# Kernel tuning notes

Hardware: AMD Instinct MI355X
Metric: run time of the kernel (lower is better)

## Reference

```python
import jax, jax.numpy as jnp
import numpy as np

B, SIZE, E = 256, 64, 4096
DEPTH = 2
ADDITIONAL = 16


def _forward(input, keys, offset, sampled_bits):
    b, s, e = input.shape
    m = SIZE >> DEPTH  # section size at this depth
    # choices: first row = round(offset), rest = sampled bits  -> (b, n, s)
    first = jax.lax.stop_gradient(jnp.round(offset)).astype(jnp.int32)[:, None, :]
    choices = jnp.concatenate([first, sampled_bits.astype(jnp.int32)], axis=1)
    n = choices.shape[1]
    # probability of each full choice vector: prod_i (offset_i if c_i else 1-offset_i)
    off = offset[:, None, :]  # (b,1,s)
    p = jnp.where(choices == 1, off, 1.0 - off)  # (b,n,s)
    probs = jnp.prod(p, axis=2, keepdims=True)  # (b,n,1)
    probs = probs / jnp.sum(probs, axis=1, keepdims=True)
    probs = jnp.broadcast_to(probs, (b, n, s))
    # util.split: element at position i (section sec, in-section pos pin) goes to
    # top half (pin//2) or bottom half (m//2 + pin//2) of its section.
    i = jnp.arange(s)
    sec = (i // m) * m
    pin = i % m
    out0 = sec + pin // 2
    out1 = sec + m // 2 + pin // 2
    indices = jnp.where(choices == 1, out1[None, None, :], out0[None, None, :])  # (b,n,s)
    # duplicates: choice rows determine index rows bijectively, so compare choice rows.
    # mark all occurrences except the first (matches stable-sort-based dedup).
    eq = jnp.all(choices[:, :, None, :] == choices[:, None, :, :], axis=-1)  # (b,n,n)
    earlier = jnp.triu(jnp.ones((n, n), dtype=bool), 1)  # mask_{i,j}: i < j
    dups = jnp.any(eq & earlier[None], axis=1)  # (b,n)
    probs = jnp.where(dups[:, :, None], 0.0, probs)
    # batched sparse matmul via dense scatter of the (s,s) matrix per batch
    rows = indices.reshape(b, -1)  # (b, n*s)
    cols = jnp.broadcast_to(i[None, None, :], (b, n, s)).reshape(b, -1)
    vals = probs.reshape(b, -1).astype(input.dtype)
    bidx = jnp.arange(b)[:, None]
    M = jnp.zeros((b, s, s), input.dtype).at[bidx, rows, cols].add(vals)  # (b,s,s)
    output = jnp.einsum('brc,bce->bre', M, input)  # (b,s,e)
    keys_out = jnp.einsum('brc,bc->br', M, keys)   # (b,s)
    return output, keys_out


def setup_inputs() -> dict:
    key = jax.random.key(0)
    k1, k2, k3, k4 = jax.random.split(key, 4)
    return {
        'input': jax.random.normal(k1, (B, SIZE, E), jnp.float32),
        'keys': jax.random.normal(k2, (B, SIZE), jnp.float32),
        'offset': jax.random.uniform(k3, (B, SIZE), jnp.float32),
        'sampled_bits': jax.random.randint(k4, (B, ADDITIONAL, SIZE), 0, 2, jnp.int32),
    }


def reference(input, keys, offset, sampled_bits):
    return _forward(input, keys, offset, sampled_bits)
```

## Files before the change

### kernel.cpp

```cpp
#include <hip/hip_runtime.h>

#define BB     256
#define S      64
#define EE     4096
#define NROWS  17

typedef float f32x4 __attribute__((ext_vector_type(4)));

__global__ __launch_bounds__(64) void split_weights_kernel(
    const float* __restrict__ keys,
    const float* __restrict__ offset,
    const int*   __restrict__ bits,
    float* __restrict__ W0,
    float* __restrict__ W1,
    float* __restrict__ keys_out)
{
    const int b    = blockIdx.x;
    const int lane = threadIdx.x;

    __shared__ float              s_off[S];
    __shared__ unsigned long long s_mask[NROWS];
    __shared__ float              s_prob[NROWS];
    __shared__ float              s_W0[S], s_W1[S];
    __shared__ float              s_sum;

    const float off = offset[b * S + lane];
    s_off[lane] = off;

    unsigned long long m = __ballot((int)rintf(off) == 1);
    if (lane == 0) s_mask[0] = m;
    for (int j = 0; j < NROWS - 1; ++j) {
        const int bit = bits[((size_t)b * (NROWS - 1) + j) * S + lane];
        m = __ballot(bit == 1);
        if (lane == 0) s_mask[1 + j] = m;
    }
    __syncthreads();

    if (lane < NROWS) {
        const unsigned long long mk = s_mask[lane];
        float p = 1.0f;
        #pragma unroll
        for (int i = 0; i < S; ++i) {
            const float o = s_off[i];
            p *= ((mk >> i) & 1ull) ? o : (1.0f - o);
        }
        s_prob[lane] = p;
    }
    __syncthreads();

    if (lane == 0) {
        float sum = 0.0f;
        #pragma unroll
        for (int j = 0; j < NROWS; ++j) sum += s_prob[j];
        s_sum = sum;
    }
    __syncthreads();

    if (lane < NROWS) {
        const unsigned long long mk = s_mask[lane];
        bool dup = false;
        for (int k = 0; k < lane; ++k) dup |= (s_mask[k] == mk);
        s_prob[lane] = dup ? 0.0f : (s_prob[lane] / s_sum);
    }
    __syncthreads();

    {
        float w0 = 0.0f, w1 = 0.0f;
        #pragma unroll
        for (int j = 0; j < NROWS; ++j) {
            const float p = s_prob[j];
            if ((s_mask[j] >> lane) & 1ull) w1 += p; else w0 += p;
        }
        s_W0[lane] = w0;
        s_W1[lane] = w1;
        W0[b * S + lane] = w0;
        W1[b * S + lane] = w1;
    }
    __syncthreads();

    {
        const int loc = lane & 15;
        const int sec = lane & ~15;
        const int t   = loc >> 3;
        const int q   = loc & 7;
        const int c0  = sec + 2 * q;
        const int c1  = c0 + 1;
        const float wa = t ? s_W1[c0] : s_W0[c0];
        const float wb = t ? s_W1[c1] : s_W0[c1];
        keys_out[b * S + lane] = wa * keys[b * S + c0] + wb * keys[b * S + c1];
    }
}

__global__ __launch_bounds__(256) void split_apply_kernel(
    const float* __restrict__ input,
    const float* __restrict__ W0,
    const float* __restrict__ W1,
    float* __restrict__ out)
{
    const int blk = blockIdx.x;
    const int b   = blk >> 5;
    const int pr  = blk & 31;
    const int sec = (pr >> 3) << 4;
    const int q   = pr & 7;
    const int c0  = sec + 2 * q;
    const int c1  = c0 + 1;
    const int r0  = sec + q;
    const int r1  = sec + 8 + q;

    const float wa0 = W0[b * S + c0], wb0 = W0[b * S + c1];
    const float wa1 = W1[b * S + c0], wb1 = W1[b * S + c1];

    const f32x4* __restrict__ in0 = (const f32x4*)(input + ((size_t)b * S + c0) * EE);
    const f32x4* __restrict__ in1 = (const f32x4*)(input + ((size_t)b * S + c1) * EE);
    f32x4* __restrict__ o0 = (f32x4*)(out + ((size_t)b * S + r0) * EE);
    f32x4* __restrict__ o1 = (f32x4*)(out + ((size_t)b * S + r1) * EE);

    const int tid = threadIdx.x;

    f32x4 x0[4], x1[4];
    #pragma unroll
    for (int it = 0; it < 4; ++it) {
        x0[it] = __builtin_nontemporal_load(&in0[tid + it * 256]);
        x1[it] = __builtin_nontemporal_load(&in1[tid + it * 256]);
    }

    #pragma unroll
    for (int it = 0; it < 4; ++it) {
        const int idx = tid + it * 256;
        f32x4 y0, y1;
        y0.x = wa0 * x0[it].x + wb0 * x1[it].x;
        y0.y = wa0 * x0[it].y + wb0 * x1[it].y;
        y0.z = wa0 * x0[it].z + wb0 * x1[it].z;
        y0.w = wa0 * x0[it].w + wb0 * x1[it].w;
        y1.x = wa1 * x0[it].x + wb1 * x1[it].x;
        y1.y = wa1 * x0[it].y + wb1 * x1[it].y;
        y1.z = wa1 * x0[it].z + wb1 * x1[it].z;
        y1.w = wa1 * x0[it].w + wb1 * x1[it].w;
        __builtin_nontemporal_store(y0, &o0[idx]);
        __builtin_nontemporal_store(y1, &o1[idx]);
    }
}

extern "C" void kernel_launch(void* const* d_in, const int* in_sizes, int n_in,
                              void* d_out, int out_size, void* d_ws, size_t ws_size,
                              hipStream_t stream) {
    const float* input  = (const float*)d_in[0];
    const float* keys   = (const float*)d_in[1];
    const float* offset = (const float*)d_in[2];
    const int*   bits   = (const int*)  d_in[3];

    float* out      = (float*)d_out;
    float* keys_out = out + (size_t)BB * S * EE;

    float* W0 = (float*)d_ws;
    float* W1 = W0 + BB * S;

    split_weights_kernel<<<BB, 64, 0, stream>>>(keys, offset, bits, W0, W1, keys_out);
    split_apply_kernel<<<BB * 32, 256, 0, stream>>>(input, W0, W1, out);
}
```

Measured before the change: 96.15 us.

## Rewrite weights kernel with register masks and wavefront shuffle reductions

Replaces the shared-memory, barrier-separated weight computation with a single-wavefront register implementation. The bit loads are batched up front, the per-row probability products use butterfly xor-shuffle reductions across all 64 lanes instead of a 64-step serial loop on 17 lanes, and the final weights reach the keys stage through shuffles. This removes __syncthreads and LDS round trips from the small prologue kernel. The large apply kernel is unchanged, so the effect on total time is bounded by the prologue's share, and the shuffle product may round differently from the serial product.

```diff
diff --git a/kernel.cpp b/kernel.cpp
--- a/kernel.cpp
+++ b/kernel.cpp
@@ -18,77 +18,64 @@
     const int b    = blockIdx.x;
     const int lane = threadIdx.x;
 
-    __shared__ float              s_off[S];
-    __shared__ unsigned long long s_mask[NROWS];
-    __shared__ float              s_prob[NROWS];
-    __shared__ float              s_W0[S], s_W1[S];
-    __shared__ float              s_sum;
+    const float off = offset[b * S + lane];
+    int bitv[16];
+    #pragma unroll
+    for (int j = 0; j < 16; ++j)
+        bitv[j] = bits[((size_t)b * 16 + j) * S + lane];
 
-    const float off = offset[b * S + lane];
-    s_off[lane] = off;
+    const int loc = lane & 15;
+    const int sec = lane & ~15;
+    const int t   = loc >> 3;
+    const int q   = loc & 7;
+    const int c0  = sec + 2 * q;
+    const int c1  = c0 + 1;
+    const float k0 = keys[b * S + c0];
+    const float k1 = keys[b * S + c1];
 
-    unsigned long long m = __ballot((int)rintf(off) == 1);
-    if (lane == 0) s_mask[0] = m;
-    for (int j = 0; j < NROWS - 1; ++j) {
-        const int bit = bits[((size_t)b * (NROWS - 1) + j) * S + lane];
-        m = __ballot(bit == 1);
-        if (lane == 0) s_mask[1 + j] = m;
+    unsigned long long mask[NROWS];
+    mask[0] = __ballot((int)rintf(off) == 1);
+    #pragma unroll
+    for (int j = 0; j < 16; ++j)
+        mask[1 + j] = __ballot(bitv[j] == 1);
+
+    const float one_m_off = 1.0f - off;
+    float prob[NROWS];
+    #pragma unroll
+    for (int j = 0; j < NROWS; ++j) {
+        float v = ((mask[j] >> lane) & 1ull) ? off : one_m_off;
+        #pragma unroll
+        for (int d = 1; d < 64; d <<= 1)
+            v *= __shfl_xor(v, d, 64);
+        prob[j] = v;
     }
-    __syncthreads();
 
-    if (lane < NROWS) {
-        const unsigned long long mk = s_mask[lane];
-        float p = 1.0f;
+    float sum = 0.0f;
+    #pragma unroll
+    for (int j = 0; j < NROWS; ++j) sum += prob[j];
+    const float inv = 1.0f / sum;
+    #pragma unroll
+    for (int j = 0; j < NROWS; ++j) {
+        bool dup = false;
         #pragma unroll
-        for (int i = 0; i < S; ++i) {
-            const float o = s_off[i];
-            p *= ((mk >> i) & 1ull) ? o : (1.0f - o);
-        }
-        s_prob[lane] = p;
+        for (int k = 0; k < NROWS; ++k)
+            if (k < j) dup |= (mask[k] == mask[j]);
+        prob[j] = dup ? 0.0f : prob[j] * inv;
     }
-    __syncthreads();
 
-    if (lane == 0) {
-        float sum = 0.0f;
-        #pragma unroll
-        for (int j = 0; j < NROWS; ++j) sum += s_prob[j];
-        s_sum = sum;
+    float w0 = 0.0f, w1 = 0.0f;
+    #pragma unroll
+    for (int j = 0; j < NROWS; ++j) {
+        if ((mask[j] >> lane) & 1ull) w1 += prob[j]; else w0 += prob[j];
     }
-    __syncthreads();
+    W0[b * S + lane] = w0;
+    W1[b * S + lane] = w1;
 
-    if (lane < NROWS) {
-        const unsigned long long mk = s_mask[lane];
-        bool dup = false;
-        for (int k = 0; k < lane; ++k) dup |= (s_mask[k] == mk);
-        s_prob[lane] = dup ? 0.0f : (s_prob[lane] / s_sum);
-    }
-    __syncthreads();
-
-    {
-        float w0 = 0.0f, w1 = 0.0f;
-        #pragma unroll
-        for (int j = 0; j < NROWS; ++j) {
-            const float p = s_prob[j];
-            if ((s_mask[j] >> lane) & 1ull) w1 += p; else w0 += p;
-        }
-        s_W0[lane] = w0;
-        s_W1[lane] = w1;
-        W0[b * S + lane] = w0;
-        W1[b * S + lane] = w1;
-    }
-    __syncthreads();
-
-    {
-        const int loc = lane & 15;
-        const int sec = lane & ~15;
-        const int t   = loc >> 3;
-        const int q   = loc & 7;
-        const int c0  = sec + 2 * q;
-        const int c1  = c0 + 1;
-        const float wa = t ? s_W1[c0] : s_W0[c0];
-        const float wb = t ? s_W1[c1] : s_W0[c1];
-        keys_out[b * S + lane] = wa * keys[b * S + c0] + wb * keys[b * S + c1];
-    }
+    const float wa0 = __shfl(w0, c0, 64), wa1 = __shfl(w1, c0, 64);
+    const float wb0 = __shfl(w0, c1, 64), wb1 = __shfl(w1, c1, 64);
+    const float wa = t ? wa1 : wa0;
+    const float wb = t ? wb1 : wb0;
+    keys_out[b * S + lane] = wa * k0 + wb * k1;
 }
 
 __global__ __launch_bounds__(256) void split_apply_kernel(
```

New measurement: 95.28 us. No clear change (-0.9%).
